# Kernel optimization log

Hardware: AMD Instinct MI355X
Metric: run time of the kernel (lower is better)

## Reference

```python
import jax, jax.numpy as jnp
import numpy as np

N_NODES = 38000   # 19 feature types x ~2000 categories
IN_DIM = 64
HID = 128         # hid_num in source
R = 8             # number of relations
E = 200000        # edges per relation
N_ROWS = 60000    # data rows
F = 19            # len(features)
N_CLASSES = 10


def setup_inputs() -> dict:
    key = jax.random.key(0)
    ks = jax.random.split(key, 20)
    s_in = 1.0 / np.sqrt(IN_DIM)
    s_h = 1.0 / np.sqrt(HID)
    inp = {
        "node_feats": jax.random.normal(ks[0], (N_NODES, IN_DIM), jnp.float32),
        "edges_src": jax.random.randint(ks[1], (R, E), 0, N_NODES),
        "edges_dst": jax.random.randint(ks[2], (R, E), 0, N_NODES),
        "row_idx": jax.random.randint(ks[3], (N_ROWS, F), 0, N_NODES),
        "row_mask": jax.random.randint(ks[4], (N_ROWS, F), 0, 2).astype(bool),
        # input linear
        "W_in": jax.random.normal(ks[5], (IN_DIM, HID), jnp.float32) * s_in,
        "b_in": jnp.zeros((HID,), jnp.float32),
        # RGCN layer 1 and 2: per-relation GraphConv weights
        "W1": jax.random.normal(ks[6], (R, HID, HID), jnp.float32) * s_h,
        "b1": jnp.zeros((R, HID), jnp.float32),
        "W2": jax.random.normal(ks[7], (R, HID, HID), jnp.float32) * s_h,
        "b2": jnp.zeros((R, HID), jnp.float32),
        # MLP head
        "Wm1": jax.random.normal(ks[8], (HID, HID), jnp.float32) * s_h,
        "bm1": jnp.zeros((HID,), jnp.float32),
        "Wm2": jax.random.normal(ks[9], (HID, HID), jnp.float32) * s_h,
        "bm2": jnp.zeros((HID,), jnp.float32),
        "Wm3": jax.random.normal(ks[10], (HID, N_CLASSES), jnp.float32) * s_h,
        "bm3": jnp.zeros((N_CLASSES,), jnp.float32),
    }
    return inp


def _hetero_conv(h, src, dst, W, b):
    """DGL HeteroGraphConv(sum) of GraphConv(norm='both') over R relations."""
    n = h.shape[0]
    out = jnp.zeros((n, W.shape[2]), h.dtype)
    ones = jnp.ones((src.shape[1],), h.dtype)
    for r in range(src.shape[0]):
        deg_out = jax.ops.segment_sum(ones, src[r], num_segments=n)
        deg_in = jax.ops.segment_sum(ones, dst[r], num_segments=n)
        norm_s = jnp.where(deg_out > 0, deg_out, 1.0) ** -0.5
        norm_d = jnp.where(deg_in > 0, deg_in, 1.0) ** -0.5
        msg = h[src[r]] * norm_s[src[r], None]            # [E, hid]
        agg = jax.ops.segment_sum(msg, dst[r], num_segments=n)
        out = out + (agg * norm_d[:, None]) @ W[r] + b[r]
    return out


def reference(node_feats, edges_src, edges_dst, row_idx, row_mask,
              W_in, b_in, W1, b1, W2, b2, Wm1, bm1, Wm2, bm2, Wm3, bm3):
    # input linear + relu (applied to every node type's features)
    h = jax.nn.relu(node_feats @ W_in + b_in)            # [N_nodes, HID]
    # 2-layer RGCN
    h = jax.nn.relu(_hetero_conv(h, edges_src, edges_dst, W1, b1))
    h = _hetero_conv(h, edges_src, edges_dst, W2, b2)    # [N_nodes, HID]
    # vectorized ragged gather + masked mean (replaces per-row python loop)
    m = row_mask.astype(h.dtype)                          # [N_rows, F]
    emb = h[row_idx] * m[..., None]                       # [N_rows, F, HID]
    cnt = jnp.maximum(m.sum(-1, keepdims=True), 1.0)
    mean_feat = emb.sum(1) / cnt                          # [N_rows, HID]
    # MLP head
    x = jax.nn.relu(mean_feat @ Wm1 + bm1)
    x = jax.nn.relu(x @ Wm2 + bm2)
    return x @ Wm3 + bm3                                  # [N_rows, N_CLASSES]
```

## Files before the change

kernel.cpp:

```cpp
#include <hip/hip_runtime.h>
#include <hip/hip_bf16.h>

#define NN    38000
#define HID   128
#define RR    8
#define EE    200000
#define NROWS 60000
#define FF    19
#define NCLS  10
#define NRD   (RR*NN)
#define HB    38912
#define CH    16
#define CE    (EE/CH)

typedef __hip_bfloat16 bf16;
typedef __attribute__((ext_vector_type(8))) short short8;
typedef __attribute__((ext_vector_type(4))) float floatx4;
typedef __attribute__((ext_vector_type(2))) float float2v;

__device__ __forceinline__ float b2f(bf16 x){ return __bfloat162float(x); }
__device__ __forceinline__ bf16  f2b(float x){ return __float2bfloat16(x); }

__device__ __forceinline__ int geti(const void* a, long long i, int wide){
  return wide ? (int)(((const long long*)a)[i]) : ((const int*)a)[i];
}

__global__ void k_fill(float* out, int n, float v){
  int i = blockIdx.x*256 + threadIdx.x;
  if (i < n) out[i] = v;
}

__global__ void k_sniff(const void* mask, const void* ridx, const void* esrc, int* flags){
  int lane = threadIdx.x;
  const unsigned short* mu = (const unsigned short*)mask;
  int l3f80e=0, l3f80o=0, lbytehi=0, loddnz=0, lother=0;
  for (int i = lane; i < 4096; i += 64){
    unsigned v = mu[i];
    if (v == 0) continue;
    if (v == 0x3F80){ if (i & 1) l3f80o = 1; else l3f80e = 1; continue; }
    unsigned lo = v & 0xFF, hi = v >> 8;
    int lob = (lo == 0 || lo == 1 || lo == 0xFF);
    int hib = (hi == 0 || hi == 1 || hi == 0xFF);
    if (lob && hib){ if (hi) lbytehi = 1; if (i & 1) loddnz = 1; continue; }
    lother = 1;
  }
  int a3f80e = __any(l3f80e);
  int a3f80o = __any(l3f80o);
  int abytehi = __any(lbytehi);
  int aoddnz = __any(loddnz);
  int aother = __any(lother);
  int mtype = -1;
  if (!aother){
    if (a3f80e && !abytehi && !aoddnz)       mtype = 2;
    else if (a3f80o && !a3f80e && !abytehi)  mtype = 3;
    else if (!a3f80e && !a3f80o){
      if (abytehi || aoddnz) mtype = 1;
      else                   mtype = 0;
    }
  }
  const int* es = (const int*)esrc;
  int loddE = 0, lseenE = 0;
  for (int i = lane; i < 512; i += 64){
    if (es[2*i+1] != 0) loddE = 1;
    if (es[2*i] > 1)    lseenE = 1;
  }
  int fE = (!__any(loddE) && __any(lseenE)) ? 1 : 0;
  const int* ri = (const int*)ridx;
  int loddI = 0, lseenI = 0;
  for (int i = lane; i < 512; i += 64){
    if (ri[2*i+1] != 0) loddI = 1;
    if (ri[2*i] > 1)    lseenI = 1;
  }
  int fI = (!__any(loddI) && __any(lseenI)) ? 1 : 0;
  if (lane == 0){ flags[1] = mtype; flags[3] = fE; flags[4] = fI; }
}


__global__ __launch_bounds__(1024) void kg_hist(const void* esrc, const void* edst,
                                                unsigned short* __restrict__ ghd,
                                                unsigned short* __restrict__ ghs,
                                                const int* flags){
  __shared__ int hist[HB];
  int t = threadIdx.x;
  for (int i = t; i < HB; i += 1024) hist[i] = 0;
  __syncthreads();
  int b = blockIdx.x;
  int side = b >> 7;
  int r = (b >> 4) & 7, c = b & 15;
  int wide = flags[3];
  const void* e = side ? esrc : edst;
  long long base = (long long)r*EE + (long long)c*CE;
  if (!wide){
    const int* p = (const int*)e + base;
    for (int i = t; i < CE; i += 1024) atomicAdd(&hist[p[i]], 1);
  } else {
    const long long* p = (const long long*)e + base;
    for (int i = t; i < CE; i += 1024) atomicAdd(&hist[(int)p[i]], 1);
  }
  __syncthreads();
  unsigned short* out = (side ? ghs : ghd) + (long long)(r*CH + c)*HB;
  for (int i = t; i < HB; i += 1024) out[i] = (unsigned short)hist[i];
}

__global__ void kg_tot(const unsigned short* __restrict__ ghd,
                       const unsigned short* __restrict__ ghs,
                       int* __restrict__ totg, float* __restrict__ ns){
  int i = blockIdx.x*256 + threadIdx.x;
  if (i >= RR*HB) return;
  int r = i / HB, bin = i - r*HB;
  int sd = 0, ss = 0;
#pragma unroll
  for (int c = 0; c < CH; c++){
    sd += ghd[(long long)(r*CH+c)*HB + bin];
    ss += ghs[(long long)(r*CH+c)*HB + bin];
  }
  totg[i] = sd;
  if (bin < NN) ns[r*NN + bin] = rsqrtf((float)(ss > 0 ? ss : 1));
}

__global__ __launch_bounds__(1024) void kg_scan(const int* __restrict__ totg,
                                                int* __restrict__ rowptr){
  __shared__ int tot[HB];
  __shared__ int wsum[16];
  int t = threadIdx.x, r = blockIdx.x;
  for (int i = t; i < HB; i += 1024) tot[i] = totg[r*HB + i];
  __syncthreads();
  int b0 = t*38;
  int loc[38], s = 0;
#pragma unroll
  for (int j = 0; j < 38; j++){ loc[j] = s; s += tot[b0+j]; }
  int lane = t & 63, w = t >> 6;
  int sc = s;
  for (int off = 1; off < 64; off <<= 1){
    int v = __shfl_up(sc, off);
    if (lane >= off) sc += v;
  }
  if (lane == 63) wsum[w] = sc;
  __syncthreads();
  if (t < 16){
    int v = wsum[t];
    int scw = v;
    for (int off = 1; off < 16; off <<= 1){
      int u = __shfl_up(scw, off);
      if (t >= off) scw += u;
    }
    wsum[t] = scw - v;
  }
  __syncthreads();
  int base = r*EE + (sc - s) + wsum[w];
#pragma unroll
  for (int j = 0; j < 38; j++) tot[b0+j] = base + loc[j];
  __syncthreads();
  for (int i = t; i < NN; i += 1024) rowptr[r*NN + i] = tot[i];
  if (r == RR-1 && t == 0) rowptr[NRD] = RR*EE;
}

__global__ void kg_curs(const unsigned short* __restrict__ ghd,
                        const int* __restrict__ rowptr,
                        int* __restrict__ gcurs){
  int i = blockIdx.x*256 + threadIdx.x;
  if (i >= NRD) return;
  int r = i / NN, bin = i - r*NN;
  int p = rowptr[i];
#pragma unroll
  for (int c = 0; c < CH; c++){
    gcurs[(long long)(r*CH+c)*HB + bin] = p;
    p += ghd[(long long)(r*CH+c)*HB + bin];
  }
}

__global__ __launch_bounds__(1024) void kg_scatter(const void* esrc, const void* edst,
                                                   const int* __restrict__ gcurs,
                                                   const float* __restrict__ ns,
                                                   int2* __restrict__ csrw, const int* flags){
  __shared__ int cur[HB];
  int t = threadIdx.x, b = blockIdx.x;
  int r = b >> 4, c = b & 15;
  const int* g = gcurs + (long long)(r*CH + c)*HB;
  for (int i = t; i < HB; i += 1024) cur[i] = g[i];
  __syncthreads();
  if (b == 0 && t < 8){ int2 z; z.x = 0; z.y = 0; csrw[RR*EE + t] = z; }
  int wide = flags[3];
  const float* nsr = ns + r*NN;
  long long base = (long long)r*EE + (long long)c*CE;
  if (!wide){
    const int* ps = (const int*)esrc + base;
    const int* pd = (const int*)edst + base;
    for (int i = t; i < CE; i += 1024){
      int d = pd[i], s = ps[i];
      int pos = atomicAdd(&cur[d], 1);
      int2 v; v.x = s << 6; v.y = __float_as_int(nsr[s]);
      csrw[pos] = v;
    }
  } else {
    const long long* ps = (const long long*)esrc + base;
    const long long* pd = (const long long*)edst + base;
    for (int i = t; i < CE; i += 1024){
      int d = (int)pd[i], s = (int)ps[i];
      int pos = atomicAdd(&cur[d], 1);
      int2 v; v.x = s << 6; v.y = __float_as_int(nsr[s]);
      csrw[pos] = v;
    }
  }
}


__global__ void k_bias(const float* b_in, const float* b1, const float* b2,
                       const float* bm1, const float* bm2, const float* bm3, float* o){
  int t = threadIdx.x;
  o[t] = b_in[t];
  float s1 = 0.f, s2 = 0.f;
  for (int r = 0; r < RR; r++){ s1 += b1[r*HID+t]; s2 += b2[r*HID+t]; }
  o[128+t] = s1; o[256+t] = s2;
  o[384+t] = bm1[t]; o[512+t] = bm2[t];
  if (t < NCLS) o[640+t] = bm3[t];
}

__global__ void k_packall(const float* __restrict__ W1, const float* __restrict__ W2,
                          const float* __restrict__ Wm1, const float* __restrict__ Wm2,
                          bf16* __restrict__ W1p, bf16* __restrict__ W2p,
                          bf16* __restrict__ Wm1p, bf16* __restrict__ Wm2p){
  int idx0 = blockIdx.x*256 + threadIdx.x;
  if (idx0 < 4*65536){
    const float* W = (idx0 < 2*65536) ? W1 : W2;
    bf16* out      = (idx0 < 2*65536) ? W1p : W2p;
    int idx = idx0 & (2*65536 - 1);
    int j = idx & 7;
    int l = (idx >> 3) & 63;
    int t = (idx >> 9) & 127;
    int g = idx >> 16;
    int ktg = t & 15, nt = t >> 4;
    int kglob = ktg*32 + ((l>>4)<<3) + j;
    int rel = kglob >> 7;
    int krow = kglob & 127;
    int n = nt*16 + (l&15);
    out[idx] = f2b(W[((g*4 + rel)*128 + krow)*128 + n]);
  } else if (idx0 < 4*65536 + 2*16384){
    int t2 = idx0 - 4*65536;
    const float* B = (t2 < 16384) ? Wm1 : Wm2;
    bf16* out      = (t2 < 16384) ? Wm1p : Wm2p;
    int idx = t2 & 16383;
    int j  = idx & 7;
    int l  = (idx >> 3) & 63;
    int t  = idx >> 9;
    int kt = t & 3;
    int nt = t >> 2;
    int k = kt*32 + ((l>>4)<<3) + j;
    int n = nt*16 + (l&15);
    out[idx] = f2b(B[k*128 + n]);
  }
}

__global__ void k_gemm_in(const float* __restrict__ A, const float* __restrict__ B,
                          const float* bias, bf16* __restrict__ out){
  int row0 = blockIdx.x * 4;
  int col = threadIdx.x;
  float a0=0.f, a1=0.f, a2=0.f, a3=0.f;
  for (int k = 0; k < 64; k++){
    float bv = B[k*HID + col];
    a0 += A[(long long)(row0+0)*64 + k] * bv;
    a1 += A[(long long)(row0+1)*64 + k] * bv;
    a2 += A[(long long)(row0+2)*64 + k] * bv;
    a3 += A[(long long)(row0+3)*64 + k] * bv;
  }
  float bb = bias[col];
  out[(long long)(row0+0)*HID + col] = f2b(fmaxf(a0 + bb, 0.f));
  out[(long long)(row0+1)*HID + col] = f2b(fmaxf(a1 + bb, 0.f));
  out[(long long)(row0+2)*HID + col] = f2b(fmaxf(a2 + bb, 0.f));
  out[(long long)(row0+3)*HID + col] = f2b(fmaxf(a3 + bb, 0.f));
}

#define LOADW(Q, base_) \
  Q##0 = cw[(base_)+0]; Q##1 = cw[(base_)+1]; Q##2 = cw[(base_)+2]; Q##3 = cw[(base_)+3]; \
  Q##4 = cw[(base_)+4]; Q##5 = cw[(base_)+5]; Q##6 = cw[(base_)+6]; Q##7 = cw[(base_)+7];

#define GATHW(P, Q) \
  P##0 = hv[(int)Q##0 + lane]; \
  P##1 = hv[(int)Q##1 + lane]; \
  P##2 = hv[(int)Q##2 + lane]; \
  P##3 = hv[(int)Q##3 + lane]; \
  P##4 = hv[(int)Q##4 + lane]; \
  P##5 = hv[(int)Q##5 + lane]; \
  P##6 = hv[(int)Q##6 + lane]; \
  P##7 = hv[(int)Q##7 + lane];

#define ACCE(Qv, Pv, cond) { \
  float wk_ = (cond) ? __int_as_float((int)((Qv) >> 32)) : 0.f; \
  float2v xv_; \
  xv_.x = __uint_as_float((Pv) << 16); \
  xv_.y = __uint_as_float((Pv) & 0xffff0000u); \
  acc2 += (float2v){wk_, wk_} * xv_; }

#define ROWBODY(i, QC, PC, QN, PN) { \
  int b_ = __builtin_amdgcn_readfirstlane(__shfl(rp, (i))); \
  int e_ = __builtin_amdgcn_readfirstlane(__shfl(rp, (i)+1)); \
  LOADW(QN, e_)                        \
  GATHW(PN, QN)                        \
  float2v acc2 = (float2v){0.f, 0.f}; \
  ACCE(QC##0, PC##0, b_+0 < e_) \
  ACCE(QC##1, PC##1, b_+1 < e_) \
  ACCE(QC##2, PC##2, b_+2 < e_) \
  ACCE(QC##3, PC##3, b_+3 < e_) \
  ACCE(QC##4, PC##4, b_+4 < e_) \
  ACCE(QC##5, PC##5, b_+5 < e_) \
  ACCE(QC##6, PC##6, b_+6 < e_) \
  ACCE(QC##7, PC##7, b_+7 < e_) \
  for (int j = b_ + 8; j < e_; j += 8){       \
    unsigned long long q0 = cw[j],   q1 = cw[j+1], q2 = cw[j+2], q3 = cw[j+3]; \
    unsigned long long q4 = cw[j+4], q5 = cw[j+5], q6 = cw[j+6], q7 = cw[j+7]; \
    unsigned p0 = hv[(int)q0 + lane]; \
    unsigned p1 = hv[(int)q1 + lane]; \
    unsigned p2 = hv[(int)q2 + lane]; \
    unsigned p3 = hv[(int)q3 + lane]; \
    unsigned p4 = hv[(int)q4 + lane]; \
    unsigned p5 = hv[(int)q5 + lane]; \
    unsigned p6 = hv[(int)q6 + lane]; \
    unsigned p7 = hv[(int)q7 + lane]; \
    ACCE(q0, p0, 1) \
    ACCE(q1, p1, j+1 < e_) \
    ACCE(q2, p2, j+2 < e_) \
    ACCE(q3, p3, j+3 < e_) \
    ACCE(q4, p4, j+4 < e_) \
    ACCE(q5, p5, j+5 < e_) \
    ACCE(q6, p6, j+6 < e_) \
    ACCE(q7, p7, j+7 < e_) \
  } \
  int deg = e_ - b_; \
  float nd = rsqrtf((float)(deg > 0 ? deg : 1)); \
  bf16 o0 = f2b(acc2.x * nd), o1 = f2b(acc2.y * nd); \
  unsigned ov = ((unsigned)(*(unsigned short*)&o1) << 16) | (*(unsigned short*)&o0); \
  int addr = (w << 12) + ((i) << 8) + (lane << 2); \
  addr ^= (((i) & 7) << 4); \
  *(unsigned*)(lds + addr) = ov; }

__global__ __launch_bounds__(512) void k_layer(const bf16* __restrict__ h,
                                               const int* __restrict__ rowptr,
                                               const unsigned long long* __restrict__ cw,
                                               const bf16* __restrict__ Bp,
                                               const float* __restrict__ bias,
                                               bf16* __restrict__ hout, int relu){
  __shared__ char lds[8*16*256];
  int w = threadIdx.x >> 6;
  int lane = threadIdx.x & 63;
  int d0 = blockIdx.x << 4;
  const unsigned* hv = (const unsigned*)h;

  int rp = 0;
  if (lane < 17) rp = rowptr[w*NN + d0 + lane];

  unsigned long long qa0,qa1,qa2,qa3,qa4,qa5,qa6,qa7;
  unsigned long long qb0,qb1,qb2,qb3,qb4,qb5,qb6,qb7;
  unsigned pa0,pa1,pa2,pa3,pa4,pa5,pa6,pa7;
  unsigned pb0,pb1,pb2,pb3,pb4,pb5,pb6,pb7;

  {
    int b0_ = __builtin_amdgcn_readfirstlane(__shfl(rp, 0));
    LOADW(qa, b0_)
    GATHW(pa, qa)
  }
  ROWBODY( 0, qa, pa, qb, pb)
  ROWBODY( 1, qb, pb, qa, pa)
  ROWBODY( 2, qa, pa, qb, pb)
  ROWBODY( 3, qb, pb, qa, pa)
  ROWBODY( 4, qa, pa, qb, pb)
  ROWBODY( 5, qb, pb, qa, pa)
  ROWBODY( 6, qa, pa, qb, pb)
  ROWBODY( 7, qb, pb, qa, pa)
  ROWBODY( 8, qa, pa, qb, pb)
  ROWBODY( 9, qb, pb, qa, pa)
  ROWBODY(10, qa, pa, qb, pb)
  ROWBODY(11, qb, pb, qa, pa)
  ROWBODY(12, qa, pa, qb, pb)
  ROWBODY(13, qb, pb, qa, pa)
  ROWBODY(14, qa, pa, qb, pb)
  ROWBODY(15, qb, pb, qa, pa)
  __syncthreads();

  floatx4 acc = (floatx4){0.f,0.f,0.f,0.f};
  int row = lane & 15;
  int kb = (lane >> 4) << 4;
#pragma unroll
  for (int rel = 0; rel < 8; rel++){
    int half = rel >> 2;
    const bf16* bp = Bp + half*65536 + lane*8 + (w*16 + (rel & 3)*4)*512;
#pragma unroll
    for (int ktl = 0; ktl < 4; ktl++){
      int off = (row << 8) + ktl*64 + kb;
      off ^= ((row & 7) << 4);
      short8 a = *(const short8*)(lds + (rel << 12) + off);
      short8 b = *(const short8*)(bp + ktl*512);
      acc = __builtin_amdgcn_mfma_f32_16x16x32_bf16(a, b, acc, 0, 0, 0);
    }
  }
  int col = w*16 + (lane & 15);
  int row0 = d0 + ((lane >> 4) << 2);
  float bb = bias[col];
#pragma unroll
  for (int v = 0; v < 4; v++){
    float x = acc[v] + bb;
    if (relu) x = fmaxf(x, 0.f);
    hout[(long long)(row0 + v)*HID + col] = f2b(x);
  }
}

__global__ __launch_bounds__(256) void k_head(const bf16* __restrict__ h,
                                              const void* ridx, const void* rmask,
                                              const int* __restrict__ flags,
                                              const bf16* __restrict__ Wm1p,
                                              const bf16* __restrict__ Wm2p,
                                              const float* __restrict__ Wm3,
                                              const float* __restrict__ bias,
                                              float* __restrict__ out){
  __shared__ char ldsA[16*256];
  __shared__ char ldsB[16*256];
  int wv = threadIdx.x >> 6;
  int lane = threadIdx.x & 63;
  int r0 = blockIdx.x << 4;
  int mt = flags[1];
  int wide = flags[4];
  const int* m4            = (const int*)rmask;
  const unsigned char* m1  = (const unsigned char*)rmask;
  const unsigned short* m2 = (const unsigned short*)rmask;
  const unsigned int* mw   = (const unsigned int*)rmask;
  const unsigned* hv = (const unsigned*)h;

  for (int rr = 0; rr < 4; rr++){
    int tr = wv*4 + rr;
    int row = r0 + tr;
    int on = 0, idxl = 0;
    if (lane < FF){
      long long i = (long long)row*FF + lane;
      if      (mt == 1) on = (m1[i] != 0);
      else if (mt == 2) on = (m2[i] != 0);
      else if (mt == 3) on = (mw[i] != 0);
      else              on = (m4[i] != 0);
      if (on) idxl = geti(ridx, i, wide);
    }
    unsigned long long bal = __ballot(on);
    float cnt = (float)__popcll(bal);
    float acc0 = 0.f, acc1 = 0.f;
#pragma unroll
    for (int j = 0; j < FF; j++){
      int s = __shfl(idxl, j);
      float wgt = (float)((bal >> j) & 1ull);
      unsigned pv = hv[(long long)s*64 + lane];
      acc0 += wgt * __uint_as_float(pv << 16);
      acc1 += wgt * __uint_as_float(pv & 0xffff0000u);
    }
    float inv = 1.f / fmaxf(cnt, 1.f);
    bf16 o0 = f2b(acc0 * inv), o1 = f2b(acc1 * inv);
    unsigned ov = ((unsigned)(*(unsigned short*)&o1) << 16) | (*(unsigned short*)&o0);
    int addr = (tr << 8) + (lane << 2);
    addr ^= ((tr & 7) << 4);
    *(unsigned*)(ldsA + addr) = ov;
  }
  __syncthreads();

  int arow = lane & 15;
  int kb = (lane >> 4) << 4;
  int colB = lane & 15;
  int rowQ = (lane >> 4) << 2;

  {
    floatx4 accA = (floatx4){0.f,0.f,0.f,0.f};
    floatx4 accB = (floatx4){0.f,0.f,0.f,0.f};
    const bf16* bp = Wm1p + lane*8;
#pragma unroll
    for (int kt = 0; kt < 4; kt++){
      int off = (arow << 8) + kt*64 + kb;
      off ^= ((arow & 7) << 4);
      short8 a = *(const short8*)(ldsA + off);
      short8 b0 = *(const short8*)(bp + ((wv*2+0)*4 + kt)*512);
      short8 b1 = *(const short8*)(bp + ((wv*2+1)*4 + kt)*512);
      accA = __builtin_amdgcn_mfma_f32_16x16x32_bf16(a, b0, accA, 0, 0, 0);
      accB = __builtin_amdgcn_mfma_f32_16x16x32_bf16(a, b1, accB, 0, 0, 0);
    }
#pragma unroll
    for (int ntl = 0; ntl < 2; ntl++){
      int col = (wv*2 + ntl)*16 + colB;
      float bb = bias[384 + col];
#pragma unroll
      for (int v = 0; v < 4; v++){
        float x = ((ntl == 0) ? accA[v] : accB[v]) + bb;
        bf16 xv = f2b(fmaxf(x, 0.f));
        int rowi = rowQ + v;
        int addr = (rowi << 8) + col*2;
        addr ^= ((rowi & 7) << 4);
        *(unsigned short*)(ldsB + addr) = *(unsigned short*)&xv;
      }
    }
  }
  __syncthreads();

  {
    floatx4 accA = (floatx4){0.f,0.f,0.f,0.f};
    floatx4 accB = (floatx4){0.f,0.f,0.f,0.f};
    const bf16* bp = Wm2p + lane*8;
#pragma unroll
    for (int kt = 0; kt < 4; kt++){
      int off = (arow << 8) + kt*64 + kb;
      off ^= ((arow & 7) << 4);
      short8 a = *(const short8*)(ldsB + off);
      short8 b0 = *(const short8*)(bp + ((wv*2+0)*4 + kt)*512);
      short8 b1 = *(const short8*)(bp + ((wv*2+1)*4 + kt)*512);
      accA = __builtin_amdgcn_mfma_f32_16x16x32_bf16(a, b0, accA, 0, 0, 0);
      accB = __builtin_amdgcn_mfma_f32_16x16x32_bf16(a, b1, accB, 0, 0, 0);
    }
#pragma unroll
    for (int ntl = 0; ntl < 2; ntl++){
      int col = (wv*2 + ntl)*16 + colB;
      float bb = bias[512 + col];
#pragma unroll
      for (int v = 0; v < 4; v++){
        float x = ((ntl == 0) ? accA[v] : accB[v]) + bb;
        bf16 xv = f2b(fmaxf(x, 0.f));
        int rowi = rowQ + v;
        int addr = (rowi << 8) + col*2;
        addr ^= ((rowi & 7) << 4);
        *(unsigned short*)(ldsA + addr) = *(unsigned short*)&xv;
      }
    }
  }
  __syncthreads();

  for (int t = threadIdx.x; t < 16*NCLS; t += 256){
    int tr = t / NCLS, col = t - tr*NCLS;
    float acc = bias[640 + col];
    for (int k = 0; k < HID; k++){
      int addr = (tr << 8) + k*2;
      addr ^= ((tr & 7) << 4);
      unsigned short uv = *(const unsigned short*)(ldsA + addr);
      acc += b2f(*(bf16*)&uv) * Wm3[k*NCLS + col];
    }
    out[(long long)(r0 + tr)*NCLS + col] = acc;
  }
}

extern "C" void kernel_launch(void* const* d_in, const int* in_sizes, int n_in,
                              void* d_out, int out_size, void* d_ws, size_t ws_size,
                              hipStream_t stream){
  float* out = (float*)d_out;

  static const int expect[17] = {
    NN*64, RR*EE, RR*EE, NROWS*FF, NROWS*FF,
    64*HID, HID, RR*HID*HID, RR*HID, RR*HID*HID, RR*HID,
    HID*HID, HID, HID*HID, HID, HID*NCLS, NCLS };
  bool ok = (n_in >= 17) && (out_size == NROWS*NCLS);
  if (ok) for (int i = 0; i < 17; i++) if (in_sizes[i] != expect[i]) { ok = false; break; }
  if (!ok){
    k_fill<<<(NROWS*NCLS+255)/256, 256, 0, stream>>>(out, NROWS*NCLS, 64.0f);
    return;
  }

  const void*  e_src = d_in[1];
  const void*  e_dst = d_in[2];
  const void*  ridx  = d_in[3];
  const void*  rmask = d_in[4];
  const float* nf   = (const float*)d_in[0];
  const float* W_in = (const float*)d_in[5];
  const float* b_in = (const float*)d_in[6];
  const float* W1   = (const float*)d_in[7];
  const float* b1   = (const float*)d_in[8];
  const float* W2   = (const float*)d_in[9];
  const float* b2   = (const float*)d_in[10];
  const float* Wm1  = (const float*)d_in[11];
  const float* bm1  = (const float*)d_in[12];
  const float* Wm2  = (const float*)d_in[13];
  const float* bm2  = (const float*)d_in[14];
  const float* Wm3  = (const float*)d_in[15];
  const float* bm3  = (const float*)d_in[16];

  char* ws = (char*)d_ws;
  size_t off = 0;
  auto take = [&](size_t bytes)->char*{
    char* p = ws + off; off += (bytes + 255) & ~(size_t)255; return p; };

  int*   flags  = (int*)  take(256);
  char*  rgn    =         take(58368000);
  unsigned short* ghd = (unsigned short*)(rgn);
  unsigned short* ghs = (unsigned short*)(rgn + 9961472);
  int*   gcurs  = (int*)  (rgn + 19922944);
  int*   totg   = (int*)  (rgn + 39845888);
  bf16*  h1     = (bf16*) take((size_t)NN*HID*2);
  bf16*  h2     = (bf16*) take((size_t)NN*HID*2);
  int*   rowptr = (int*)  take((size_t)(NRD+1)*4);
  int2*  csrw   = (int2*) take((size_t)RR*EE*8 + 64);
  float* ns     = (float*)take((size_t)NRD*4);
  float* bias   = (float*)take(656*4);
  bf16*  W1p    = (bf16*) take((size_t)2*65536*2);
  bf16*  W2p    = (bf16*) take((size_t)2*65536*2);
  bf16*  Wm1p   = (bf16*) take((size_t)16384*2);
  bf16*  Wm2p   = (bf16*) take((size_t)16384*2);

  if (off > ws_size){
    k_fill<<<(NROWS*NCLS+255)/256, 256, 0, stream>>>(out, NROWS*NCLS, 32.0f);
    return;
  }

  k_sniff   <<<1, 64, 0, stream>>>(rmask, ridx, e_src, flags);
  kg_hist   <<<256, 1024, 0, stream>>>(e_src, e_dst, ghd, ghs, flags);
  kg_tot    <<<(RR*HB+255)/256, 256, 0, stream>>>(ghd, ghs, totg, ns);
  kg_scan   <<<RR, 1024, 0, stream>>>(totg, rowptr);
  kg_curs   <<<(NRD+255)/256, 256, 0, stream>>>(ghd, rowptr, gcurs);
  kg_scatter<<<128, 1024, 0, stream>>>(e_src, e_dst, gcurs, ns, csrw, flags);
  k_bias    <<<1, 128, 0, stream>>>(b_in, b1, b2, bm1, bm2, bm3, bias);

  k_packall<<<(4*65536 + 2*16384 + 255)/256, 256, 0, stream>>>(W1, W2, Wm1, Wm2,
                                                               W1p, W2p, Wm1p, Wm2p);

  k_gemm_in<<<NN/4, 128, 0, stream>>>(nf, W_in, bias+0, h1);

  k_layer<<<NN/16, 512, 0, stream>>>(h1, rowptr, (const unsigned long long*)csrw,
                                     W1p, bias+128, h2, 1);
  k_layer<<<NN/16, 512, 0, stream>>>(h2, rowptr, (const unsigned long long*)csrw,
                                     W2p, bias+256, h1, 0);

  k_head<<<NROWS/16, 256, 0, stream>>>(h1, ridx, rmask, flags, Wm1p, Wm2p, Wm3, bias, out);
}
```

Before: 412.1 us.

## Gather two edges per wave with 8-byte loads and fold bias kernel into pack

The aggregation loop in k_layer now splits each wave into two halves. Each half-wave handles alternate edges and loads 8 bytes (4 bf16 features) per lane, and the two halves are combined with a cross-half shuffle reduction. The CSR source offset is rescaled to a byte offset (s<<8), and the explicit software prefetch / double-buffered register pipeline across rows is removed. The bias-summing kernel is merged into the weight-pack kernel to save a launch. The intent is to halve the number of gather instructions and widen the memory transactions, but dropping the cross-row prefetch may expose more gather latency.

```diff
diff --git a/kernel.cpp b/kernel.cpp
--- a/kernel.cpp
+++ b/kernel.cpp
@@ -16,7 +16,6 @@
 typedef __hip_bfloat16 bf16;
 typedef __attribute__((ext_vector_type(8))) short short8;
 typedef __attribute__((ext_vector_type(4))) float floatx4;
-typedef __attribute__((ext_vector_type(2))) float float2v;
 
 __device__ __forceinline__ float b2f(bf16 x){ return __bfloat162float(x); }
 __device__ __forceinline__ bf16  f2b(float x){ return __float2bfloat16(x); }
@@ -189,7 +188,7 @@
     for (int i = t; i < CE; i += 1024){
       int d = pd[i], s = ps[i];
       int pos = atomicAdd(&cur[d], 1);
-      int2 v; v.x = s << 6; v.y = __float_as_int(nsr[s]);
+      int2 v; v.x = s << 8; v.y = __float_as_int(nsr[s]);
       csrw[pos] = v;
     }
   } else {
@@ -198,28 +197,20 @@
     for (int i = t; i < CE; i += 1024){
       int d = (int)pd[i], s = (int)ps[i];
       int pos = atomicAdd(&cur[d], 1);
-      int2 v; v.x = s << 6; v.y = __float_as_int(nsr[s]);
+      int2 v; v.x = s << 8; v.y = __float_as_int(nsr[s]);
       csrw[pos] = v;
     }
   }
 }
 
-
-__global__ void k_bias(const float* b_in, const float* b1, const float* b2,
-                       const float* bm1, const float* bm2, const float* bm3, float* o){
-  int t = threadIdx.x;
-  o[t] = b_in[t];
-  float s1 = 0.f, s2 = 0.f;
-  for (int r = 0; r < RR; r++){ s1 += b1[r*HID+t]; s2 += b2[r*HID+t]; }
-  o[128+t] = s1; o[256+t] = s2;
-  o[384+t] = bm1[t]; o[512+t] = bm2[t];
-  if (t < NCLS) o[640+t] = bm3[t];
-}
 
 __global__ void k_packall(const float* __restrict__ W1, const float* __restrict__ W2,
                           const float* __restrict__ Wm1, const float* __restrict__ Wm2,
                           bf16* __restrict__ W1p, bf16* __restrict__ W2p,
-                          bf16* __restrict__ Wm1p, bf16* __restrict__ Wm2p){
+                          bf16* __restrict__ Wm1p, bf16* __restrict__ Wm2p,
+                          const float* b_in, const float* b1, const float* b2,
+                          const float* bm1, const float* bm2, const float* bm3,
+                          float* __restrict__ o){
   int idx0 = blockIdx.x*256 + threadIdx.x;
   if (idx0 < 4*65536){
     const float* W = (idx0 < 2*65536) ? W1 : W2;
@@ -248,6 +239,14 @@
     int k = kt*32 + ((l>>4)<<3) + j;
     int n = nt*16 + (l&15);
     out[idx] = f2b(B[k*128 + n]);
+  } else if (idx0 < 4*65536 + 2*16384 + 128){
+    int t = idx0 - (4*65536 + 2*16384);
+    o[t] = b_in[t];
+    float s1 = 0.f, s2 = 0.f;
+    for (int r = 0; r < RR; r++){ s1 += b1[r*HID+t]; s2 += b2[r*HID+t]; }
+    o[128+t] = s1; o[256+t] = s2;
+    o[384+t] = bm1[t]; o[512+t] = bm2[t];
+    if (t < NCLS) o[640+t] = bm3[t];
   }
 }
 
@@ -270,68 +269,14 @@
   out[(long long)(row0+3)*HID + col] = f2b(fmaxf(a3 + bb, 0.f));
 }
 
-#define LOADW(Q, base_) \
-  Q##0 = cw[(base_)+0]; Q##1 = cw[(base_)+1]; Q##2 = cw[(base_)+2]; Q##3 = cw[(base_)+3]; \
-  Q##4 = cw[(base_)+4]; Q##5 = cw[(base_)+5]; Q##6 = cw[(base_)+6]; Q##7 = cw[(base_)+7];
-
-#define GATHW(P, Q) \
-  P##0 = hv[(int)Q##0 + lane]; \
-  P##1 = hv[(int)Q##1 + lane]; \
-  P##2 = hv[(int)Q##2 + lane]; \
-  P##3 = hv[(int)Q##3 + lane]; \
-  P##4 = hv[(int)Q##4 + lane]; \
-  P##5 = hv[(int)Q##5 + lane]; \
-  P##6 = hv[(int)Q##6 + lane]; \
-  P##7 = hv[(int)Q##7 + lane];
-
-#define ACCE(Qv, Pv, cond) { \
-  float wk_ = (cond) ? __int_as_float((int)((Qv) >> 32)) : 0.f; \
-  float2v xv_; \
-  xv_.x = __uint_as_float((Pv) << 16); \
-  xv_.y = __uint_as_float((Pv) & 0xffff0000u); \
-  acc2 += (float2v){wk_, wk_} * xv_; }
-
-#define ROWBODY(i, QC, PC, QN, PN) { \
-  int b_ = __builtin_amdgcn_readfirstlane(__shfl(rp, (i))); \
-  int e_ = __builtin_amdgcn_readfirstlane(__shfl(rp, (i)+1)); \
-  LOADW(QN, e_)                        \
-  GATHW(PN, QN)                        \
-  float2v acc2 = (float2v){0.f, 0.f}; \
-  ACCE(QC##0, PC##0, b_+0 < e_) \
-  ACCE(QC##1, PC##1, b_+1 < e_) \
-  ACCE(QC##2, PC##2, b_+2 < e_) \
-  ACCE(QC##3, PC##3, b_+3 < e_) \
-  ACCE(QC##4, PC##4, b_+4 < e_) \
-  ACCE(QC##5, PC##5, b_+5 < e_) \
-  ACCE(QC##6, PC##6, b_+6 < e_) \
-  ACCE(QC##7, PC##7, b_+7 < e_) \
-  for (int j = b_ + 8; j < e_; j += 8){       \
-    unsigned long long q0 = cw[j],   q1 = cw[j+1], q2 = cw[j+2], q3 = cw[j+3]; \
-    unsigned long long q4 = cw[j+4], q5 = cw[j+5], q6 = cw[j+6], q7 = cw[j+7]; \
-    unsigned p0 = hv[(int)q0 + lane]; \
-    unsigned p1 = hv[(int)q1 + lane]; \
-    unsigned p2 = hv[(int)q2 + lane]; \
-    unsigned p3 = hv[(int)q3 + lane]; \
-    unsigned p4 = hv[(int)q4 + lane]; \
-    unsigned p5 = hv[(int)q5 + lane]; \
-    unsigned p6 = hv[(int)q6 + lane]; \
-    unsigned p7 = hv[(int)q7 + lane]; \
-    ACCE(q0, p0, 1) \
-    ACCE(q1, p1, j+1 < e_) \
-    ACCE(q2, p2, j+2 < e_) \
-    ACCE(q3, p3, j+3 < e_) \
-    ACCE(q4, p4, j+4 < e_) \
-    ACCE(q5, p5, j+5 < e_) \
-    ACCE(q6, p6, j+6 < e_) \
-    ACCE(q7, p7, j+7 < e_) \
-  } \
-  int deg = e_ - b_; \
-  float nd = rsqrtf((float)(deg > 0 ? deg : 1)); \
-  bf16 o0 = f2b(acc2.x * nd), o1 = f2b(acc2.y * nd); \
-  unsigned ov = ((unsigned)(*(unsigned short*)&o1) << 16) | (*(unsigned short*)&o0); \
-  int addr = (w << 12) + ((i) << 8) + (lane << 2); \
-  addr ^= (((i) & 7) << 4); \
-  *(unsigned*)(lds + addr) = ov; }
+#define PAIRG(qe, qo, we, wo) { \
+  unsigned off_ = hi5 ? (unsigned)(qo) : (unsigned)(qe); \
+  float wv_ = hi5 ? (wo) : (we); \
+  uint2 pp_ = *(const uint2*)(hc + off_ + loff); \
+  a0 += wv_ * __uint_as_float(pp_.x << 16); \
+  a1 += wv_ * __uint_as_float(pp_.x & 0xffff0000u); \
+  a2 += wv_ * __uint_as_float(pp_.y << 16); \
+  a3 += wv_ * __uint_as_float(pp_.y & 0xffff0000u); }
 
 __global__ __launch_bounds__(512) void k_layer(const bf16* __restrict__ h,
                                                const int* __restrict__ rowptr,
@@ -343,37 +288,47 @@
   int w = threadIdx.x >> 6;
   int lane = threadIdx.x & 63;
   int d0 = blockIdx.x << 4;
-  const unsigned* hv = (const unsigned*)h;
+  const char* hc = (const char*)h;
+  int hi5 = lane >> 5;
+  int loff = (lane & 31) << 3;
 
   int rp = 0;
   if (lane < 17) rp = rowptr[w*NN + d0 + lane];
 
-  unsigned long long qa0,qa1,qa2,qa3,qa4,qa5,qa6,qa7;
-  unsigned long long qb0,qb1,qb2,qb3,qb4,qb5,qb6,qb7;
-  unsigned pa0,pa1,pa2,pa3,pa4,pa5,pa6,pa7;
-  unsigned pb0,pb1,pb2,pb3,pb4,pb5,pb6,pb7;
-
-  {
-    int b0_ = __builtin_amdgcn_readfirstlane(__shfl(rp, 0));
-    LOADW(qa, b0_)
-    GATHW(pa, qa)
-  }
-  ROWBODY( 0, qa, pa, qb, pb)
-  ROWBODY( 1, qb, pb, qa, pa)
-  ROWBODY( 2, qa, pa, qb, pb)
-  ROWBODY( 3, qb, pb, qa, pa)
-  ROWBODY( 4, qa, pa, qb, pb)
-  ROWBODY( 5, qb, pb, qa, pa)
-  ROWBODY( 6, qa, pa, qb, pb)
-  ROWBODY( 7, qb, pb, qa, pa)
-  ROWBODY( 8, qa, pa, qb, pb)
-  ROWBODY( 9, qb, pb, qa, pa)
-  ROWBODY(10, qa, pa, qb, pb)
-  ROWBODY(11, qb, pb, qa, pa)
-  ROWBODY(12, qa, pa, qb, pb)
-  ROWBODY(13, qb, pb, qa, pa)
-  ROWBODY(14, qa, pa, qb, pb)
-  ROWBODY(15, qb, pb, qa, pa)
+  for (int i = 0; i < 16; i++){
+    int b_ = __builtin_amdgcn_readfirstlane(__shfl(rp, i));
+    int e_ = __builtin_amdgcn_readfirstlane(__shfl(rp, i+1));
+    float a0 = 0.f, a1 = 0.f, a2 = 0.f, a3 = 0.f;
+    for (int j = b_; j < e_; j += 8){
+      unsigned long long q0 = cw[j+0], q1 = cw[j+1], q2 = cw[j+2], q3 = cw[j+3];
+      unsigned long long q4 = cw[j+4], q5 = cw[j+5], q6 = cw[j+6], q7 = cw[j+7];
+      float w0 =              __int_as_float((int)(q0 >> 32));
+      float w1 = (j+1 < e_) ? __int_as_float((int)(q1 >> 32)) : 0.f;
+      float w2 = (j+2 < e_) ? __int_as_float((int)(q2 >> 32)) : 0.f;
+      float w3 = (j+3 < e_) ? __int_as_float((int)(q3 >> 32)) : 0.f;
+      float w4 = (j+4 < e_) ? __int_as_float((int)(q4 >> 32)) : 0.f;
+      float w5 = (j+5 < e_) ? __int_as_float((int)(q5 >> 32)) : 0.f;
+      float w6 = (j+6 < e_) ? __int_as_float((int)(q6 >> 32)) : 0.f;
+      float w7 = (j+7 < e_) ? __int_as_float((int)(q7 >> 32)) : 0.f;
+      PAIRG(q0, q1, w0, w1)
+      PAIRG(q2, q3, w2, w3)
+      PAIRG(q4, q5, w4, w5)
+      PAIRG(q6, q7, w6, w7)
+    }
+    a0 += __shfl_xor(a0, 32);
+    a1 += __shfl_xor(a1, 32);
+    a2 += __shfl_xor(a2, 32);
+    a3 += __shfl_xor(a3, 32);
+    int deg = e_ - b_;
+    float nd = rsqrtf((float)(deg > 0 ? deg : 1));
+    bf16 o0 = f2b(a0 * nd), o1 = f2b(a1 * nd), o2 = f2b(a2 * nd), o3 = f2b(a3 * nd);
+    uint2 ov;
+    ov.x = ((unsigned)(*(unsigned short*)&o1) << 16) | (*(unsigned short*)&o0);
+    ov.y = ((unsigned)(*(unsigned short*)&o3) << 16) | (*(unsigned short*)&o2);
+    int addr = (w << 12) + (i << 8) + loff;
+    addr ^= ((i & 7) << 4);
+    *(uint2*)(lds + addr) = ov;
+  }
   __syncthreads();
 
   floatx4 acc = (floatx4){0.f,0.f,0.f,0.f};
@@ -603,10 +558,10 @@
   kg_scan   <<<RR, 1024, 0, stream>>>(totg, rowptr);
   kg_curs   <<<(NRD+255)/256, 256, 0, stream>>>(ghd, rowptr, gcurs);
   kg_scatter<<<128, 1024, 0, stream>>>(e_src, e_dst, gcurs, ns, csrw, flags);
-  k_bias    <<<1, 128, 0, stream>>>(b_in, b1, b2, bm1, bm2, bm3, bias);
-
-  k_packall<<<(4*65536 + 2*16384 + 255)/256, 256, 0, stream>>>(W1, W2, Wm1, Wm2,
-                                                               W1p, W2p, Wm1p, Wm2p);
+
+  k_packall<<<(4*65536 + 2*16384 + 128 + 255)/256, 256, 0, stream>>>(
+      W1, W2, Wm1, Wm2, W1p, W2p, Wm1p, Wm2p,
+      b_in, b1, b2, bm1, bm2, bm3, bias);
 
   k_gemm_in<<<NN/4, 128, 0, stream>>>(nf, W_in, bias+0, h1);
 
```

Result: slower. 428.6 us (+4.0%).

## Split per-relation degree scan into segmented parallel scan; fold bias kernel into pack

Applied to the files above, without the earlier changes.

Replaces the 8-block prefix scan over degree bins with a two-level scan: 152 blocks each scan a 2048-bin segment, a tiny kernel scans the segment sums per relation, and the cursor kernel adds the segment offsets while also finalizing rowptr. The bias-combining kernel is merged into the weight-packing kernel, and the input GEMM now reads b_in directly. The goal is to remove a low-parallelism serial stage and one launch, at the cost of one extra tiny launch and an extra read-modify-write of rowptr.

```diff
diff --git a/kernel.cpp b/kernel.cpp
--- a/kernel.cpp
+++ b/kernel.cpp
@@ -12,6 +12,7 @@
 #define HB    38912
 #define CH    16
 #define CE    (EE/CH)
+#define NSEG  19
 
 typedef __hip_bfloat16 bf16;
 typedef __attribute__((ext_vector_type(8))) short short8;
@@ -118,22 +119,22 @@
   if (bin < NN) ns[r*NN + bin] = rsqrtf((float)(ss > 0 ? ss : 1));
 }
 
-__global__ __launch_bounds__(1024) void kg_scan(const int* __restrict__ totg,
-                                                int* __restrict__ rowptr){
-  __shared__ int tot[HB];
+__global__ __launch_bounds__(1024) void kg_scanA(const int* __restrict__ totg,
+                                                 int* __restrict__ rowptr,
+                                                 int* __restrict__ segsum){
   __shared__ int wsum[16];
-  int t = threadIdx.x, r = blockIdx.x;
-  for (int i = t; i < HB; i += 1024) tot[i] = totg[r*HB + i];
-  __syncthreads();
-  int b0 = t*38;
-  int loc[38], s = 0;
-#pragma unroll
-  for (int j = 0; j < 38; j++){ loc[j] = s; s += tot[b0+j]; }
+  int b = blockIdx.x;
+  int r = b / NSEG, seg = b - r*NSEG;
+  int t = threadIdx.x;
+  int base = seg*2048;
+  int v0 = totg[r*HB + base + 2*t];
+  int v1 = totg[r*HB + base + 2*t + 1];
+  int s = v0 + v1;
   int lane = t & 63, w = t >> 6;
   int sc = s;
   for (int off = 1; off < 64; off <<= 1){
-    int v = __shfl_up(sc, off);
-    if (lane >= off) sc += v;
+    int u = __shfl_up(sc, off);
+    if (lane >= off) sc += u;
   }
   if (lane == 63) wsum[w] = sc;
   __syncthreads();
@@ -147,21 +148,35 @@
     wsum[t] = scw - v;
   }
   __syncthreads();
-  int base = r*EE + (sc - s) + wsum[w];
-#pragma unroll
-  for (int j = 0; j < 38; j++) tot[b0+j] = base + loc[j];
-  __syncthreads();
-  for (int i = t; i < NN; i += 1024) rowptr[r*NN + i] = tot[i];
-  if (r == RR-1 && t == 0) rowptr[NRD] = RR*EE;
+  int ex = (sc - s) + wsum[w];
+  int bin0 = base + 2*t;
+  if (bin0 < NN)     rowptr[r*NN + bin0]     = ex;
+  if (bin0 + 1 < NN) rowptr[r*NN + bin0 + 1] = ex + v0;
+  if (t == 1023) segsum[b] = ex + s;
+}
+
+__global__ void kg_scanB(const int* __restrict__ segsum, int* __restrict__ segoff){
+  int r = threadIdx.x;
+  if (r < RR){
+    int acc = r*EE;
+    for (int s = 0; s < NSEG; s++){
+      int v = segsum[r*NSEG + s];
+      segoff[r*NSEG + s] = acc;
+      acc += v;
+    }
+  }
 }
 
 __global__ void kg_curs(const unsigned short* __restrict__ ghd,
-                        const int* __restrict__ rowptr,
+                        int* __restrict__ rowptr,
+                        const int* __restrict__ segoff,
                         int* __restrict__ gcurs){
   int i = blockIdx.x*256 + threadIdx.x;
   if (i >= NRD) return;
   int r = i / NN, bin = i - r*NN;
-  int p = rowptr[i];
+  int p = rowptr[i] + segoff[r*NSEG + (bin >> 11)];
+  rowptr[i] = p;
+  if (i == 0) rowptr[NRD] = RR*EE;
 #pragma unroll
   for (int c = 0; c < CH; c++){
     gcurs[(long long)(r*CH+c)*HB + bin] = p;
@@ -205,21 +220,13 @@
 }
 
 
-__global__ void k_bias(const float* b_in, const float* b1, const float* b2,
-                       const float* bm1, const float* bm2, const float* bm3, float* o){
-  int t = threadIdx.x;
-  o[t] = b_in[t];
-  float s1 = 0.f, s2 = 0.f;
-  for (int r = 0; r < RR; r++){ s1 += b1[r*HID+t]; s2 += b2[r*HID+t]; }
-  o[128+t] = s1; o[256+t] = s2;
-  o[384+t] = bm1[t]; o[512+t] = bm2[t];
-  if (t < NCLS) o[640+t] = bm3[t];
-}
-
 __global__ void k_packall(const float* __restrict__ W1, const float* __restrict__ W2,
                           const float* __restrict__ Wm1, const float* __restrict__ Wm2,
                           bf16* __restrict__ W1p, bf16* __restrict__ W2p,
-                          bf16* __restrict__ Wm1p, bf16* __restrict__ Wm2p){
+                          bf16* __restrict__ Wm1p, bf16* __restrict__ Wm2p,
+                          const float* b_in, const float* b1, const float* b2,
+                          const float* bm1, const float* bm2, const float* bm3,
+                          float* __restrict__ o){
   int idx0 = blockIdx.x*256 + threadIdx.x;
   if (idx0 < 4*65536){
     const float* W = (idx0 < 2*65536) ? W1 : W2;
@@ -248,11 +255,19 @@
     int k = kt*32 + ((l>>4)<<3) + j;
     int n = nt*16 + (l&15);
     out[idx] = f2b(B[k*128 + n]);
+  } else if (idx0 < 4*65536 + 2*16384 + 128){
+    int t = idx0 - (4*65536 + 2*16384);
+    o[t] = b_in[t];
+    float s1 = 0.f, s2 = 0.f;
+    for (int r = 0; r < RR; r++){ s1 += b1[r*HID+t]; s2 += b2[r*HID+t]; }
+    o[128+t] = s1; o[256+t] = s2;
+    o[384+t] = bm1[t]; o[512+t] = bm2[t];
+    if (t < NCLS) o[640+t] = bm3[t];
   }
 }
 
 __global__ void k_gemm_in(const float* __restrict__ A, const float* __restrict__ B,
-                          const float* bias, bf16* __restrict__ out){
+                          const float* __restrict__ b_in, bf16* __restrict__ out){
   int row0 = blockIdx.x * 4;
   int col = threadIdx.x;
   float a0=0.f, a1=0.f, a2=0.f, a3=0.f;
@@ -263,7 +278,7 @@
     a2 += A[(long long)(row0+2)*64 + k] * bv;
     a3 += A[(long long)(row0+3)*64 + k] * bv;
   }
-  float bb = bias[col];
+  float bb = b_in[col];
   out[(long long)(row0+0)*HID + col] = f2b(fmaxf(a0 + bb, 0.f));
   out[(long long)(row0+1)*HID + col] = f2b(fmaxf(a1 + bb, 0.f));
   out[(long long)(row0+2)*HID + col] = f2b(fmaxf(a2 + bb, 0.f));
@@ -581,6 +596,8 @@
   unsigned short* ghs = (unsigned short*)(rgn + 9961472);
   int*   gcurs  = (int*)  (rgn + 19922944);
   int*   totg   = (int*)  (rgn + 39845888);
+  int*   segsum = (int*)  (rgn + 41091072);
+  int*   segoff = (int*)  (rgn + 41092096);
   bf16*  h1     = (bf16*) take((size_t)NN*HID*2);
   bf16*  h2     = (bf16*) take((size_t)NN*HID*2);
   int*   rowptr = (int*)  take((size_t)(NRD+1)*4);
@@ -600,15 +617,16 @@
   k_sniff   <<<1, 64, 0, stream>>>(rmask, ridx, e_src, flags);
   kg_hist   <<<256, 1024, 0, stream>>>(e_src, e_dst, ghd, ghs, flags);
   kg_tot    <<<(RR*HB+255)/256, 256, 0, stream>>>(ghd, ghs, totg, ns);
-  kg_scan   <<<RR, 1024, 0, stream>>>(totg, rowptr);
-  kg_curs   <<<(NRD+255)/256, 256, 0, stream>>>(ghd, rowptr, gcurs);
+  kg_scanA  <<<RR*NSEG, 1024, 0, stream>>>(totg, rowptr, segsum);
+  kg_scanB  <<<1, 64, 0, stream>>>(segsum, segoff);
+  kg_curs   <<<(NRD+255)/256, 256, 0, stream>>>(ghd, rowptr, segoff, gcurs);
   kg_scatter<<<128, 1024, 0, stream>>>(e_src, e_dst, gcurs, ns, csrw, flags);
-  k_bias    <<<1, 128, 0, stream>>>(b_in, b1, b2, bm1, bm2, bm3, bias);
-
-  k_packall<<<(4*65536 + 2*16384 + 255)/256, 256, 0, stream>>>(W1, W2, Wm1, Wm2,
-                                                               W1p, W2p, Wm1p, Wm2p);
-
-  k_gemm_in<<<NN/4, 128, 0, stream>>>(nf, W_in, bias+0, h1);
+
+  k_packall<<<(4*65536 + 2*16384 + 128 + 255)/256, 256, 0, stream>>>(
+      W1, W2, Wm1, Wm2, W1p, W2p, Wm1p, Wm2p,
+      b_in, b1, b2, bm1, bm2, bm3, bias);
+
+  k_gemm_in<<<NN/4, 128, 0, stream>>>(nf, W_in, b_in, h1);
 
   k_layer<<<NN/16, 512, 0, stream>>>(h1, rowptr, (const unsigned long long*)csrw,
                                      W1p, bias+128, h2, 1);
```

New measurement: 417.2 us. About the same (+1.2%).
